# Optimization experiments

Hardware: AMD Instinct MI355X
Metric: run time of the kernel (lower is better)

## Reference

```python
import jax, jax.numpy as jnp
import numpy as np

N = 100000   # nodes
E = 400000   # edges
G = 2048     # graphs in batch
H = 128      # hidden_channels
V = 100      # in_channels (element vocab)
L = 3        # hidden_layers (GAT)
LO = 2       # out_layers (dense)
SLOPE = 0.2  # GATConv negative_slope default


def setup_inputs() -> dict:
    key = jax.random.key(0)
    ks = jax.random.split(key, 14)
    s = 1.0 / np.sqrt(H)
    return {
        "x": jax.random.randint(ks[0], (N,), 0, V),
        "edge_index": jax.random.randint(ks[1], (2, E), 0, N),
        "edge_attr": jax.random.uniform(ks[2], (E, 1), dtype=jnp.float32),
        "batch": jnp.sort(jax.random.randint(ks[3], (N,), 0, G)),
        "emb": jax.random.normal(ks[4], (V, H), dtype=jnp.float32),
        "gat_W": jax.random.normal(ks[5], (L, H, H), dtype=jnp.float32) * s,
        "att_src": jax.random.normal(ks[6], (L, H), dtype=jnp.float32) * s,
        "att_dst": jax.random.normal(ks[7], (L, H), dtype=jnp.float32) * s,
        "edge_W": jax.random.normal(ks[8], (L, H), dtype=jnp.float32) * s,  # lin_edge: Linear(1, H, bias=False)
        "att_edge": jax.random.normal(ks[9], (L, H), dtype=jnp.float32) * s,
        "gat_b": jnp.zeros((L, H), dtype=jnp.float32),
        "lin_W": jax.random.normal(ks[10], (LO, H, H), dtype=jnp.float32) * s,
        "lin_b": jnp.zeros((LO, H), dtype=jnp.float32),
        "wp_W": jax.random.normal(ks[11], (H, 1), dtype=jnp.float32) * s,
        "wp_b": jnp.zeros((1,), dtype=jnp.float32),
    }


def _segment_softmax(logits, seg, num_segments):
    m = jax.ops.segment_max(logits, seg, num_segments=num_segments)
    e = jnp.exp(logits - m[seg])
    s = jax.ops.segment_sum(e, seg, num_segments=num_segments)
    return e / s[seg]


def reference(x, edge_index, edge_attr, batch, emb, gat_W, att_src, att_dst,
              edge_W, att_edge, gat_b, lin_W, lin_b, wp_W, wp_b):
    src, dst = edge_index[0], edge_index[1]
    # GATConv add_self_loops=True with fill_value='mean' for edge_attr
    loop = jnp.arange(N, dtype=src.dtype)
    src_sl = jnp.concatenate([src, loop])          # [E+N]
    dst_sl = jnp.concatenate([dst, loop])          # [E+N]
    ea_mean = jnp.mean(edge_attr, axis=0, keepdims=True)  # [1,1]
    ea_sl = jnp.concatenate([edge_attr, jnp.broadcast_to(ea_mean, (N, 1))], axis=0)  # [E+N,1]

    h = emb[x]  # [N,H]
    for l in range(L):
        xt = h @ gat_W[l]                 # shared lin_src/lin_dst, heads=1
        a_s = xt @ att_src[l]             # [N]
        a_d = xt @ att_dst[l]             # [N]
        a_e = (ea_sl * edge_W[l][None, :]) @ att_edge[l]  # lin_edge then att_edge: [E+N]
        alpha = jax.nn.leaky_relu(a_s[src_sl] + a_d[dst_sl] + a_e, negative_slope=SLOPE)
        alpha = _segment_softmax(alpha, dst_sl, N)
        out = jax.ops.segment_sum(xt[src_sl] * alpha[:, None], dst_sl, num_segments=N)
        out = out + gat_b[l]
        # F.normalize(h_x, 2, dim=1)
        nrm = jnp.linalg.norm(out, axis=1, keepdims=True)
        h = out / jnp.maximum(nrm, 1e-12)
    for i in range(LO):
        h = jax.nn.relu(h @ lin_W[i] + lin_b[i])
    m_x = jax.ops.segment_sum(h, batch, num_segments=G)  # scatter_sum readout [G,H]
    props = m_x @ wp_W + wp_b                            # [G,1]
    return jnp.squeeze(props, axis=1)                    # [G]
```

## Files before the change

kernel.cpp:

```cpp
#include <hip/hip_runtime.h>
#include <math.h>

#define N_NODES 100000
#define N_EDGES 400000
#define NG 2048
#define H 128
#define NV 100
#define NLAYERS 3
#define SLOPE 0.2f

#define SCAL_N 64

typedef __attribute__((ext_vector_type(8))) short bf16x8;
typedef __attribute__((ext_vector_type(4))) float f32x4;

__device__ __forceinline__ float wave_reduce_sum(float v){
  #pragma unroll
  for (int off = 32; off > 0; off >>= 1) v += __shfl_xor(v, off, 64);
  return v;
}
__device__ __forceinline__ unsigned short bfhi(float f){
  return (unsigned short)(__float_as_uint(f) >> 16);
}
__device__ __forceinline__ float bftof(unsigned short h){
  return __uint_as_float(((unsigned int)h) << 16);
}
__device__ __forceinline__ unsigned short rne_bf16(float f){
  unsigned int u = __float_as_uint(f);
  u += 0x7FFF + ((u >> 16) & 1);
  return (unsigned short)(u >> 16);
}

#define PB_CONVW 640
#define PB_CONVE (PB_CONVW + 50)
#define PB_OUT   (PB_CONVE + 8)
#define PB_DOTS  (PB_OUT + 1)
#define PB_EASUM (PB_DOTS + 256)
#define PB_DEG   (PB_EASUM + 1954)
__global__ __launch_bounds__(256) void k_prep(
    const float* __restrict__ gat_W, const float* __restrict__ lin_W,
    unsigned short* __restrict__ Wf,
    const float* __restrict__ emb, unsigned short* __restrict__ embb,
    const float* __restrict__ ea, const float* __restrict__ ew,
    const float* __restrict__ ae, float* __restrict__ scal,
    const float* __restrict__ wp_b, float* __restrict__ out,
    const int* __restrict__ ei, int* __restrict__ deg)
{
  int b = blockIdx.x, tid = threadIdx.x;
  if (b < PB_CONVW){
    int i = b*256 + tid;
    int m   = i >> 15;
    int r   = i & 32767;
    int p   = r >> 14;
    int r2  = r & 16383;
    int k0i = r2 >> 12;
    int r3  = r2 & 4095;
    int ct  = r3 >> 9;
    int r4  = r3 & 511;
    int lane= r4 >> 3;
    int j   = r4 & 7;
    int q = lane >> 4, ln = lane & 15;
    int k = k0i*32 + q*8 + j;
    int n = ct*16 + ln;
    const float* src = (m < 3) ? (gat_W + m*16384) : (lin_W + (m-3)*16384);
    float w = src[k*H + n];
    unsigned short hi = bfhi(w);
    Wf[i] = (p == 0) ? hi : bfhi(w - bftof(hi));
  } else if (b < PB_CONVE){
    int i = (b - PB_CONVW)*256 + tid;
    if (i < NV*H) embb[i] = rne_bf16(emb[i]);
  } else if (b < PB_OUT){
    int g = (b - PB_CONVE)*256 + tid;
    if (g < NG) out[g] = wp_b[0];
  } else if (b < PB_DOTS){
    int l = tid >> 6, ln = tid & 63;
    if (l < NLAYERS){
      float p = ew[l*H + ln]*ae[l*H + ln] + ew[l*H + ln + 64]*ae[l*H + ln + 64];
      p = wave_reduce_sum(p);
      if (ln == 0) atomicAdd(&scal[32 + l], p);
    }
  } else if (b < PB_EASUM){
    int i = (b - PB_DOTS)*256 + tid;
    int stride = 256*256;
    float v = 0.f;
    for (; i < N_EDGES; i += stride) v += ea[i];
    v = wave_reduce_sum(v);
    if ((tid & 63) == 0) atomicAdd(&scal[0], v);
  } else {
    int i = (b - PB_EASUM)*256 + tid;
    if (i < N_EDGES + N_NODES){
      int d = (i < N_EDGES) ? ei[N_EDGES + i] : (i - N_EDGES);
      atomicAdd(&deg[d], 1);
    }
  }
}

__global__ __launch_bounds__(256) void k_alloc(
    const int* __restrict__ deg, int* __restrict__ row_ptr, int* __restrict__ counter){
  __shared__ int wsum[4];
  __shared__ int base;
  int n = blockIdx.x * 256 + threadIdx.x;
  int d = (n < N_NODES) ? deg[n] : 0;
  int lane = threadIdx.x & 63, wid = threadIdx.x >> 6;
  int v = d;
  #pragma unroll
  for (int off = 1; off < 64; off <<= 1){
    int u = __shfl_up(v, off, 64);
    if (lane >= off) v += u;
  }
  if (lane == 63) wsum[wid] = v;
  __syncthreads();
  if (threadIdx.x == 0){
    int t0 = wsum[0], t1 = wsum[1], t2 = wsum[2], t3 = wsum[3];
    base = atomicAdd(counter, t0 + t1 + t2 + t3);
    wsum[0] = 0; wsum[1] = t0; wsum[2] = t0 + t1; wsum[3] = t0 + t1 + t2;
  }
  __syncthreads();
  if (n < N_NODES) row_ptr[n] = base + wsum[wid] + (v - d);
}

__global__ void k_scatter(const int* __restrict__ ei, const float* __restrict__ ea,
                          const float* __restrict__ scal, const int* __restrict__ row_ptr,
                          int* __restrict__ cursor, int* __restrict__ csr_src,
                          float* __restrict__ csr_ea){
  int i = blockIdx.x * blockDim.x + threadIdx.x;
  if (i >= N_EDGES + N_NODES) return;
  int s, d; float v;
  if (i < N_EDGES){ s = ei[i]; d = ei[N_EDGES + i]; v = ea[i]; }
  else            { s = d = i - N_EDGES; v = scal[0] * (1.0f / N_EDGES); }
  int pos = row_ptr[d] + atomicAdd(&cursor[d], 1);
  csr_src[pos] = s;
  csr_ea[pos]  = v;
}

__global__ __launch_bounds__(256, 2) void k_gemm(
    const unsigned short* __restrict__ Ab, const int* __restrict__ xmap,
    const unsigned short* __restrict__ Wf,
    unsigned short* __restrict__ Cb,
    const float* __restrict__ att1, const float* __restrict__ att2,
    float* __restrict__ a_s_out, float* __restrict__ a_d_out,
    const float* __restrict__ bias,
    const int* __restrict__ batch, float* __restrict__ out,
    int mode)
{
  __shared__ unsigned short lw[32768];
  int tid  = threadIdx.x;
  int w    = tid >> 6;
  int lane = tid & 63;
  int q    = lane >> 4;
  int ln   = lane & 15;
  int waveRow = blockIdx.x*256 + w*64;

  bf16x8 af[4][4];
  #pragma unroll
  for (int m = 0; m < 4; ++m){
    int r = waveRow + m*16 + ln;
    if (r >= N_NODES) r = N_NODES - 1;
    if (xmap) r = xmap[r];
    const unsigned short* Ar = Ab + (size_t)r*H;
    #pragma unroll
    for (int k0i = 0; k0i < 4; ++k0i)
      af[m][k0i] = *(const bf16x8*)(Ar + k0i*32 + q*8);
  }

  #pragma unroll
  for (int i = 0; i < 16; ++i){
    int idx = (i*256 + tid) * 8;
    *(bf16x8*)(lw + idx) = *(const bf16x8*)(Wf + idx);
  }
  __syncthreads();

  f32x4 acc[4][8];
  #pragma unroll
  for (int m = 0; m < 4; ++m)
    #pragma unroll
    for (int ct = 0; ct < 8; ++ct) acc[m][ct] = (f32x4){0.f,0.f,0.f,0.f};

  #pragma unroll
  for (int k0i = 0; k0i < 4; ++k0i){
    #pragma unroll
    for (int ct = 0; ct < 8; ++ct){
      bf16x8 bhi = *(const bf16x8*)(lw + k0i*4096 + ct*512 + lane*8);
      bf16x8 blo = *(const bf16x8*)(lw + 16384 + k0i*4096 + ct*512 + lane*8);
      #pragma unroll
      for (int m = 0; m < 4; ++m){
        acc[m][ct] = __builtin_amdgcn_mfma_f32_16x16x32_bf16(af[m][k0i], blo, acc[m][ct], 0,0,0);
        acc[m][ct] = __builtin_amdgcn_mfma_f32_16x16x32_bf16(af[m][k0i], bhi, acc[m][ct], 0,0,0);
      }
    }
  }

  if (mode == 0){
    float as_l[8], ad_l[8];
    #pragma unroll
    for (int ct = 0; ct < 8; ++ct){ as_l[ct] = att1[ct*16+ln]; ad_l[ct] = att2[ct*16+ln]; }
    #pragma unroll
    for (int m = 0; m < 4; ++m){
      #pragma unroll
      for (int r = 0; r < 4; ++r){
        int grow = waveRow + m*16 + q*4 + r;
        bool ok = grow < N_NODES;
        float ps = 0.f, pd = 0.f;
        #pragma unroll
        for (int ct = 0; ct < 8; ++ct){
          float v = acc[m][ct][r];
          if (ok) Cb[(size_t)grow*H + ct*16 + ln] = rne_bf16(v);
          ps += v * as_l[ct]; pd += v * ad_l[ct];
        }
        #pragma unroll
        for (int mk = 8; mk > 0; mk >>= 1){
          ps += __shfl_xor(ps, mk, 64);
          pd += __shfl_xor(pd, mk, 64);
        }
        if (ok && ln == 0){ a_s_out[grow] = ps; a_d_out[grow] = pd; }
      }
    }
  } else if (mode == 1){
    float b_l[8];
    #pragma unroll
    for (int ct = 0; ct < 8; ++ct) b_l[ct] = bias[ct*16+ln];
    #pragma unroll
    for (int m = 0; m < 4; ++m){
      #pragma unroll
      for (int r = 0; r < 4; ++r){
        int grow = waveRow + m*16 + q*4 + r;
        if (grow >= N_NODES) continue;
        #pragma unroll
        for (int ct = 0; ct < 8; ++ct)
          Cb[(size_t)grow*H + ct*16 + ln] = rne_bf16(fmaxf(acc[m][ct][r] + b_l[ct], 0.f));
      }
    }
  } else {
    float b_l[8], wp_l[8];
    #pragma unroll
    for (int ct = 0; ct < 8; ++ct){ b_l[ct] = bias[ct*16+ln]; wp_l[ct] = att1[ct*16+ln]; }
    #pragma unroll
    for (int m = 0; m < 4; ++m){
      #pragma unroll
      for (int r = 0; r < 4; ++r){
        int grow = waveRow + m*16 + q*4 + r;
        bool ok = grow < N_NODES;
        float ps = 0.f;
        #pragma unroll
        for (int ct = 0; ct < 8; ++ct)
          ps += fmaxf(acc[m][ct][r] + b_l[ct], 0.f) * wp_l[ct];
        #pragma unroll
        for (int mk = 8; mk > 0; mk >>= 1) ps += __shfl_xor(ps, mk, 64);
        if (ok && ln == 0) atomicAdd(&out[batch[grow]], ps);
      }
    }
  }
}

__global__ __launch_bounds__(256, 4) void k_aggregate(
    const uint2* __restrict__ xtb2, const float* __restrict__ a_s,
    const float* __restrict__ a_d, const int* __restrict__ csr_src,
    const float* __restrict__ csr_ea, const int* __restrict__ row_ptr,
    const int* __restrict__ deg, const float* __restrict__ scal, int l,
    const float* __restrict__ bias, uint2* __restrict__ hb2)
{
  __shared__ int2 lsw[4][2][32];
  int wid  = threadIdx.x >> 6;
  int lane = threadIdx.x & 63;
  int h    = lane >> 5;
  int c    = lane & 31;
  int n    = blockIdx.x*8 + wid*2 + h;
  if (n >= N_NODES) return;
  int beg = row_ptr[n];
  int d   = deg[n];
  float adn = a_d[n];
  float dl  = scal[32 + l];
  int maxd = max(d, __shfl_xor(d, 32, 64));

  float4 acc = make_float4(0.f,0.f,0.f,0.f);
  float ss = 0.f;
  for (int base = 0; base < maxd; base += 32){
    int s = 0; float wgt = 0.f;
    int j = base + c;
    if (j < d){
      int e = beg + j;
      s = csr_src[e];
      float lg = a_s[s] + adn + dl*csr_ea[e];
      lg = (lg > 0.f) ? lg : SLOPE*lg;
      wgt = __expf(lg);
    }
    int2 pk; pk.x = s; pk.y = __float_as_int(wgt);
    lsw[wid][h][c] = pk;

    int cnt8 = (min(32, maxd - base) + 7) & ~7;
    for (int j0 = 0; j0 < cnt8; j0 += 8){
      int2 sw[8];
      #pragma unroll
      for (int u = 0; u < 8; ++u) sw[u] = lsw[wid][h][j0 + u];
      uint2 xv[8];
      #pragma unroll
      for (int u = 0; u < 8; ++u)
        xv[u] = xtb2[(size_t)sw[u].x*(H/4) + c];
      #pragma unroll
      for (int u = 0; u < 8; ++u){
        float wgt8 = __int_as_float(sw[u].y);
        float x0 = __uint_as_float(xv[u].x << 16);
        float x1 = __uint_as_float(xv[u].x & 0xFFFF0000u);
        float x2 = __uint_as_float(xv[u].y << 16);
        float x3 = __uint_as_float(xv[u].y & 0xFFFF0000u);
        ss    += wgt8;
        acc.x += wgt8 * x0;
        acc.y += wgt8 * x1;
        acc.z += wgt8 * x2;
        acc.w += wgt8 * x3;
      }
    }
  }

  float4 bv = *(const float4*)(bias + c*4);
  float inv = 1.0f / ss;
  acc.x = acc.x*inv + bv.x;
  acc.y = acc.y*inv + bv.y;
  acc.z = acc.z*inv + bv.z;
  acc.w = acc.w*inv + bv.w;
  float sq = acc.x*acc.x + acc.y*acc.y + acc.z*acc.z + acc.w*acc.w;
  #pragma unroll
  for (int off = 16; off > 0; off >>= 1) sq += __shfl_xor(sq, off, 64);
  float rn = 1.0f / fmaxf(sqrtf(sq), 1e-12f);
  uint2 o;
  o.x = ((unsigned int)rne_bf16(acc.y*rn) << 16) | rne_bf16(acc.x*rn);
  o.y = ((unsigned int)rne_bf16(acc.w*rn) << 16) | rne_bf16(acc.z*rn);
  hb2[(size_t)n*(H/4) + c] = o;
}

extern "C" void kernel_launch(void* const* d_in, const int* in_sizes, int n_in,
                              void* d_out, int out_size, void* d_ws, size_t ws_size,
                              hipStream_t stream) {
  const int*   x          = (const int*)  d_in[0];
  const int*   edge_index = (const int*)  d_in[1];
  const float* edge_attr  = (const float*)d_in[2];
  const int*   batch      = (const int*)  d_in[3];
  const float* emb        = (const float*)d_in[4];
  const float* gat_W      = (const float*)d_in[5];
  const float* att_src    = (const float*)d_in[6];
  const float* att_dst    = (const float*)d_in[7];
  const float* edge_W     = (const float*)d_in[8];
  const float* att_edge   = (const float*)d_in[9];
  const float* gat_b      = (const float*)d_in[10];
  const float* lin_W      = (const float*)d_in[11];
  const float* lin_b      = (const float*)d_in[12];
  const float* wp_W       = (const float*)d_in[13];
  const float* wp_b       = (const float*)d_in[14];
  float* out = (float*)d_out;

  unsigned short* hb  = (unsigned short*)d_ws;
  unsigned short* xtb = hb + (size_t)N_NODES*H;
  unsigned short* Wt  = xtb + (size_t)N_NODES*H;
  unsigned short* embb= Wt + 5*32768;
  float* a_s    = (float*)(embb + NV*H);
  float* a_d    = a_s + N_NODES;
  float* csr_ea = a_d + N_NODES;
  float* scal   = csr_ea + (N_EDGES + N_NODES);
  int*   deg    = (int*)(scal + SCAL_N);
  int*   cursor = deg + N_NODES;
  int*   row_ptr= cursor + N_NODES;
  int*   csr_src= row_ptr + N_NODES;

  hipMemsetAsync(scal, 0, (size_t)(SCAL_N + 2*N_NODES) * sizeof(float), stream);

  k_prep<<<PB_DEG, 256, 0, stream>>>(
      gat_W, lin_W, Wt, emb, embb, edge_attr, edge_W, att_edge, scal,
      wp_b, out, edge_index, deg);
  k_alloc<<<(N_NODES + 255)/256, 256, 0, stream>>>(deg, row_ptr, (int*)&scal[48]);
  k_scatter<<<(N_EDGES + N_NODES + 255)/256, 256, 0, stream>>>(
      edge_index, edge_attr, scal, row_ptr, cursor, csr_src, csr_ea);

  const int gemm_grid = (N_NODES + 255) / 256;
  for (int l = 0; l < NLAYERS; ++l){
    k_gemm<<<gemm_grid, 256, 0, stream>>>(
        (l == 0) ? embb : hb, (l == 0) ? x : nullptr,
        Wt + (size_t)l*32768, xtb,
        att_src + l*H, att_dst + l*H, a_s, a_d,
        nullptr, nullptr, nullptr, 0);
    k_aggregate<<<(N_NODES + 7)/8, 256, 0, stream>>>(
        (const uint2*)xtb, a_s, a_d, csr_src, csr_ea, row_ptr, deg,
        scal, l, gat_b + l*H, (uint2*)hb);
  }
  k_gemm<<<gemm_grid, 256, 0, stream>>>(
      hb, nullptr, Wt + (size_t)3*32768, xtb,
      nullptr, nullptr, nullptr, nullptr, lin_b, nullptr, nullptr, 1);
  k_gemm<<<gemm_grid, 256, 0, stream>>>(
      xtb, nullptr, Wt + (size_t)4*32768, nullptr,
      wp_W, nullptr, nullptr, nullptr, lin_b + H, batch, out, 2);
}
```

Measured before the change: 337.7 us.

## Drop split-bf16 weights, shrink GEMM tile, degree-sort nodes for aggregation

Weights are now a single RNE bf16 copy instead of a hi/lo split, which halves the MFMA count and the LDS footprint of the GEMM. The GEMM block is reduced to 128 rows and the occupancy hint is raised. A degree histogram plus a new k_perm kernel build a permutation that groups nodes by degree, so paired half-waves in the aggregate kernel have similar loop lengths. This costs some GEMM precision and adds an extra kernel and an indirection per node.

```diff
diff --git a/kernel.cpp b/kernel.cpp
--- a/kernel.cpp
+++ b/kernel.cpp
@@ -9,7 +9,7 @@
 #define NLAYERS 3
 #define SLOPE 0.2f
 
-#define SCAL_N 64
+#define SCAL_N 256
 
 typedef __attribute__((ext_vector_type(8))) short bf16x8;
 typedef __attribute__((ext_vector_type(4))) float f32x4;
@@ -18,12 +18,6 @@
   #pragma unroll
   for (int off = 32; off > 0; off >>= 1) v += __shfl_xor(v, off, 64);
   return v;
-}
-__device__ __forceinline__ unsigned short bfhi(float f){
-  return (unsigned short)(__float_as_uint(f) >> 16);
-}
-__device__ __forceinline__ float bftof(unsigned short h){
-  return __uint_as_float(((unsigned int)h) << 16);
 }
 __device__ __forceinline__ unsigned short rne_bf16(float f){
   unsigned int u = __float_as_uint(f);
@@ -31,7 +25,7 @@
   return (unsigned short)(u >> 16);
 }
 
-#define PB_CONVW 640
+#define PB_CONVW 320
 #define PB_CONVE (PB_CONVW + 50)
 #define PB_OUT   (PB_CONVE + 8)
 #define PB_DOTS  (PB_OUT + 1)
@@ -49,12 +43,10 @@
   int b = blockIdx.x, tid = threadIdx.x;
   if (b < PB_CONVW){
     int i = b*256 + tid;
-    int m   = i >> 15;
-    int r   = i & 32767;
-    int p   = r >> 14;
-    int r2  = r & 16383;
-    int k0i = r2 >> 12;
-    int r3  = r2 & 4095;
+    int m   = i >> 14;
+    int r   = i & 16383;
+    int k0i = r >> 12;
+    int r3  = r & 4095;
     int ct  = r3 >> 9;
     int r4  = r3 & 511;
     int lane= r4 >> 3;
@@ -63,9 +55,7 @@
     int k = k0i*32 + q*8 + j;
     int n = ct*16 + ln;
     const float* src = (m < 3) ? (gat_W + m*16384) : (lin_W + (m-3)*16384);
-    float w = src[k*H + n];
-    unsigned short hi = bfhi(w);
-    Wf[i] = (p == 0) ? hi : bfhi(w - bftof(hi));
+    Wf[i] = rne_bf16(src[k*H + n]);
   } else if (b < PB_CONVE){
     int i = (b - PB_CONVW)*256 + tid;
     if (i < NV*H) embb[i] = rne_bf16(emb[i]);
@@ -96,9 +86,12 @@
 }
 
 __global__ __launch_bounds__(256) void k_alloc(
-    const int* __restrict__ deg, int* __restrict__ row_ptr, int* __restrict__ counter){
+    const int* __restrict__ deg, int* __restrict__ row_ptr,
+    int* __restrict__ counter, int* __restrict__ hist){
   __shared__ int wsum[4];
   __shared__ int base;
+  __shared__ int lhist[64];
+  if (threadIdx.x < 64) lhist[threadIdx.x] = 0;
   int n = blockIdx.x * 256 + threadIdx.x;
   int d = (n < N_NODES) ? deg[n] : 0;
   int lane = threadIdx.x & 63, wid = threadIdx.x >> 6;
@@ -115,14 +108,31 @@
     base = atomicAdd(counter, t0 + t1 + t2 + t3);
     wsum[0] = 0; wsum[1] = t0; wsum[2] = t0 + t1; wsum[3] = t0 + t1 + t2;
   }
+  if (n < N_NODES) atomicAdd(&lhist[min(d, 63)], 1);
   __syncthreads();
   if (n < N_NODES) row_ptr[n] = base + wsum[wid] + (v - d);
+  if (threadIdx.x < 64 && lhist[threadIdx.x] > 0)
+    atomicAdd(&hist[threadIdx.x], lhist[threadIdx.x]);
 }
 
 __global__ void k_scatter(const int* __restrict__ ei, const float* __restrict__ ea,
                           const float* __restrict__ scal, const int* __restrict__ row_ptr,
                           int* __restrict__ cursor, int* __restrict__ csr_src,
-                          float* __restrict__ csr_ea){
+                          float* __restrict__ csr_ea,
+                          const int* __restrict__ hist, int* __restrict__ binbase){
+  if (blockIdx.x == 1954){
+    int lane = threadIdx.x;
+    if (lane < 64){
+      int v = hist[lane];
+      #pragma unroll
+      for (int off = 1; off < 64; off <<= 1){
+        int u = __shfl_up(v, off, 64);
+        if (lane >= off) v += u;
+      }
+      binbase[lane] = v - hist[lane];
+    }
+    return;
+  }
   int i = blockIdx.x * blockDim.x + threadIdx.x;
   if (i >= N_EDGES + N_NODES) return;
   int s, d; float v;
@@ -133,7 +143,29 @@
   csr_ea[pos]  = v;
 }
 
-__global__ __launch_bounds__(256, 2) void k_gemm(
+__global__ __launch_bounds__(256) void k_perm(
+    const int* __restrict__ deg, const int* __restrict__ binbase,
+    int* __restrict__ bincur, int* __restrict__ perm){
+  __shared__ int lhist[64];
+  __shared__ int lbase[64];
+  if (threadIdx.x < 64) lhist[threadIdx.x] = 0;
+  __syncthreads();
+  int n = blockIdx.x * 256 + threadIdx.x;
+  int d = 0, rank = 0;
+  if (n < N_NODES){
+    d = min(deg[n], 63);
+    rank = atomicAdd(&lhist[d], 1);
+  }
+  __syncthreads();
+  if (threadIdx.x < 64){
+    int c = lhist[threadIdx.x];
+    lbase[threadIdx.x] = (c > 0) ? atomicAdd(&bincur[threadIdx.x], c) : 0;
+  }
+  __syncthreads();
+  if (n < N_NODES) perm[binbase[d] + lbase[d] + rank] = n;
+}
+
+__global__ __launch_bounds__(256, 4) void k_gemm(
     const unsigned short* __restrict__ Ab, const int* __restrict__ xmap,
     const unsigned short* __restrict__ Wf,
     unsigned short* __restrict__ Cb,
@@ -143,17 +175,17 @@
     const int* __restrict__ batch, float* __restrict__ out,
     int mode)
 {
-  __shared__ unsigned short lw[32768];
+  __shared__ unsigned short lw[16384];
   int tid  = threadIdx.x;
   int w    = tid >> 6;
   int lane = tid & 63;
   int q    = lane >> 4;
   int ln   = lane & 15;
-  int waveRow = blockIdx.x*256 + w*64;
-
-  bf16x8 af[4][4];
-  #pragma unroll
-  for (int m = 0; m < 4; ++m){
+  int waveRow = blockIdx.x*128 + w*32;
+
+  bf16x8 af[2][4];
+  #pragma unroll
+  for (int m = 0; m < 2; ++m){
     int r = waveRow + m*16 + ln;
     if (r >= N_NODES) r = N_NODES - 1;
     if (xmap) r = xmap[r];
@@ -164,15 +196,15 @@
   }
 
   #pragma unroll
-  for (int i = 0; i < 16; ++i){
+  for (int i = 0; i < 8; ++i){
     int idx = (i*256 + tid) * 8;
     *(bf16x8*)(lw + idx) = *(const bf16x8*)(Wf + idx);
   }
   __syncthreads();
 
-  f32x4 acc[4][8];
-  #pragma unroll
-  for (int m = 0; m < 4; ++m)
+  f32x4 acc[2][8];
+  #pragma unroll
+  for (int m = 0; m < 2; ++m)
     #pragma unroll
     for (int ct = 0; ct < 8; ++ct) acc[m][ct] = (f32x4){0.f,0.f,0.f,0.f};
 
@@ -180,13 +212,10 @@
   for (int k0i = 0; k0i < 4; ++k0i){
     #pragma unroll
     for (int ct = 0; ct < 8; ++ct){
-      bf16x8 bhi = *(const bf16x8*)(lw + k0i*4096 + ct*512 + lane*8);
-      bf16x8 blo = *(const bf16x8*)(lw + 16384 + k0i*4096 + ct*512 + lane*8);
-      #pragma unroll
-      for (int m = 0; m < 4; ++m){
-        acc[m][ct] = __builtin_amdgcn_mfma_f32_16x16x32_bf16(af[m][k0i], blo, acc[m][ct], 0,0,0);
-        acc[m][ct] = __builtin_amdgcn_mfma_f32_16x16x32_bf16(af[m][k0i], bhi, acc[m][ct], 0,0,0);
-      }
+      bf16x8 bw = *(const bf16x8*)(lw + k0i*4096 + ct*512 + lane*8);
+      #pragma unroll
+      for (int m = 0; m < 2; ++m)
+        acc[m][ct] = __builtin_amdgcn_mfma_f32_16x16x32_bf16(af[m][k0i], bw, acc[m][ct], 0,0,0);
     }
   }
 
@@ -195,7 +224,7 @@
     #pragma unroll
     for (int ct = 0; ct < 8; ++ct){ as_l[ct] = att1[ct*16+ln]; ad_l[ct] = att2[ct*16+ln]; }
     #pragma unroll
-    for (int m = 0; m < 4; ++m){
+    for (int m = 0; m < 2; ++m){
       #pragma unroll
       for (int r = 0; r < 4; ++r){
         int grow = waveRow + m*16 + q*4 + r;
@@ -220,7 +249,7 @@
     #pragma unroll
     for (int ct = 0; ct < 8; ++ct) b_l[ct] = bias[ct*16+ln];
     #pragma unroll
-    for (int m = 0; m < 4; ++m){
+    for (int m = 0; m < 2; ++m){
       #pragma unroll
       for (int r = 0; r < 4; ++r){
         int grow = waveRow + m*16 + q*4 + r;
@@ -235,7 +264,7 @@
     #pragma unroll
     for (int ct = 0; ct < 8; ++ct){ b_l[ct] = bias[ct*16+ln]; wp_l[ct] = att1[ct*16+ln]; }
     #pragma unroll
-    for (int m = 0; m < 4; ++m){
+    for (int m = 0; m < 2; ++m){
       #pragma unroll
       for (int r = 0; r < 4; ++r){
         int grow = waveRow + m*16 + q*4 + r;
@@ -256,7 +285,8 @@
     const uint2* __restrict__ xtb2, const float* __restrict__ a_s,
     const float* __restrict__ a_d, const int* __restrict__ csr_src,
     const float* __restrict__ csr_ea, const int* __restrict__ row_ptr,
-    const int* __restrict__ deg, const float* __restrict__ scal, int l,
+    const int* __restrict__ deg, const int* __restrict__ perm,
+    const float* __restrict__ scal, int l,
     const float* __restrict__ bias, uint2* __restrict__ hb2)
 {
   __shared__ int2 lsw[4][2][32];
@@ -264,10 +294,11 @@
   int lane = threadIdx.x & 63;
   int h    = lane >> 5;
   int c    = lane & 31;
-  int n    = blockIdx.x*8 + wid*2 + h;
-  if (n >= N_NODES) return;
+  int idx  = blockIdx.x*8 + wid*2 + h;
+  bool live = idx < N_NODES;
+  int n = live ? perm[idx] : 0;
   int beg = row_ptr[n];
-  int d   = deg[n];
+  int d   = live ? deg[n] : 0;
   float adn = a_d[n];
   float dl  = scal[32 + l];
   int maxd = max(d, __shfl_xor(d, 32, 64));
@@ -311,6 +342,7 @@
       }
     }
   }
+  if (!live) return;
 
   float4 bv = *(const float4*)(bias + c*4);
   float inv = 1.0f / ss;
@@ -351,7 +383,7 @@
   unsigned short* hb  = (unsigned short*)d_ws;
   unsigned short* xtb = hb + (size_t)N_NODES*H;
   unsigned short* Wt  = xtb + (size_t)N_NODES*H;
-  unsigned short* embb= Wt + 5*32768;
+  unsigned short* embb= Wt + 5*16384;
   float* a_s    = (float*)(embb + NV*H);
   float* a_d    = a_s + N_NODES;
   float* csr_ea = a_d + N_NODES;
@@ -360,31 +392,39 @@
   int*   cursor = deg + N_NODES;
   int*   row_ptr= cursor + N_NODES;
   int*   csr_src= row_ptr + N_NODES;
+  int*   perm   = csr_src + (N_EDGES + N_NODES);
+
+  int*   hist    = (int*)&scal[64];
+  int*   binbase = (int*)&scal[128];
+  int*   bincur  = (int*)&scal[192];
 
   hipMemsetAsync(scal, 0, (size_t)(SCAL_N + 2*N_NODES) * sizeof(float), stream);
 
   k_prep<<<PB_DEG, 256, 0, stream>>>(
       gat_W, lin_W, Wt, emb, embb, edge_attr, edge_W, att_edge, scal,
       wp_b, out, edge_index, deg);
-  k_alloc<<<(N_NODES + 255)/256, 256, 0, stream>>>(deg, row_ptr, (int*)&scal[48]);
-  k_scatter<<<(N_EDGES + N_NODES + 255)/256, 256, 0, stream>>>(
-      edge_index, edge_attr, scal, row_ptr, cursor, csr_src, csr_ea);
-
-  const int gemm_grid = (N_NODES + 255) / 256;
+  k_alloc<<<(N_NODES + 255)/256, 256, 0, stream>>>(
+      deg, row_ptr, (int*)&scal[48], hist);
+  k_scatter<<<1955, 256, 0, stream>>>(
+      edge_index, edge_attr, scal, row_ptr, cursor, csr_src, csr_ea,
+      hist, binbase);
+  k_perm<<<(N_NODES + 255)/256, 256, 0, stream>>>(deg, binbase, bincur, perm);
+
+  const int gemm_grid = (N_NODES + 127) / 128;
   for (int l = 0; l < NLAYERS; ++l){
     k_gemm<<<gemm_grid, 256, 0, stream>>>(
         (l == 0) ? embb : hb, (l == 0) ? x : nullptr,
-        Wt + (size_t)l*32768, xtb,
+        Wt + (size_t)l*16384, xtb,
         att_src + l*H, att_dst + l*H, a_s, a_d,
         nullptr, nullptr, nullptr, 0);
     k_aggregate<<<(N_NODES + 7)/8, 256, 0, stream>>>(
-        (const uint2*)xtb, a_s, a_d, csr_src, csr_ea, row_ptr, deg,
+        (const uint2*)xtb, a_s, a_d, csr_src, csr_ea, row_ptr, deg, perm,
         scal, l, gat_b + l*H, (uint2*)hb);
   }
   k_gemm<<<gemm_grid, 256, 0, stream>>>(
-      hb, nullptr, Wt + (size_t)3*32768, xtb,
+      hb, nullptr, Wt + (size_t)3*16384, xtb,
       nullptr, nullptr, nullptr, nullptr, lin_b, nullptr, nullptr, 1);
   k_gemm<<<gemm_grid, 256, 0, stream>>>(
-      xtb, nullptr, Wt + (size_t)4*32768, nullptr,
+      xtb, nullptr, Wt + (size_t)4*16384, nullptr,
       wp_W, nullptr, nullptr, nullptr, lin_b + H, batch, out, 2);
 }
```

Result: no change. 339.3 us (+0.5%).
